# Performance work log

Measured on AMD Instinct MI355X. Metric: run time of the kernel, lower is better.

## Reference

```python
import jax, jax.numpy as jnp
import numpy as np
from jax import lax

DN = ('NCHW', 'OIHW', 'NCHW')
EPS = 1e-5


def _conv3x3(x, w, b):
    return lax.conv_general_dilated(x, w, (1, 1), 'SAME', dimension_numbers=DN) + b[:, None, None]


def _conv1x1(x, w, b):
    return jnp.einsum('bchw,oc->bohw', x, w) + b[:, None, None]


def _dwconv3x3(x, w, b):
    # w: (C,1,3,3), depthwise
    C = x.shape[1]
    return lax.conv_general_dilated(x, w, (1, 1), 'SAME', feature_group_count=C,
                                    dimension_numbers=DN) + b[:, None, None]


def setup_inputs() -> dict:
    key = jax.random.key(0)
    ks = jax.random.split(key, 24)
    b, t, c, h, w = 2, 8, 64, 160, 160
    r, K = c // 4, 3

    def n(k, shape, s=0.05):
        return jax.random.normal(k, shape, dtype=jnp.float32) * s

    return {
        'feature': n(ks[0], (b, t, c, h, w), 1.0),
        'kc_w1': n(ks[1], (r, c)),
        'kc_bn_gamma': jnp.ones((r,), jnp.float32),
        'kc_bn_beta': jnp.zeros((r,), jnp.float32),
        'kc_bn_mean': jnp.zeros((r,), jnp.float32),
        'kc_bn_var': jnp.ones((r,), jnp.float32),
        'kc_w2': n(ks[2], (c * K * K, r)),
        'kc_b2': n(ks[3], (c * K * K,)),
        'kc_bias': n(ks[4], (c,)),
        'conv1_w': n(ks[5], (2 * c, 2 * c, 3, 3)),
        'conv1_b': n(ks[6], (2 * c,)),
        'pi1_w': n(ks[7], (4 * c, c)),
        'pi1_b': n(ks[8], (4 * c,)),
        'dw1_w': n(ks[9], (4 * c, 1, 3, 3)),
        'dw1_b': n(ks[10], (4 * c,)),
        'po1_w': n(ks[11], (c, 4 * c)),
        'po1_b': n(ks[12], (c,)),
        'pi2_w': n(ks[13], (4 * c, c)),
        'pi2_b': n(ks[14], (4 * c,)),
        'dw2_w': n(ks[15], (4 * c, 1, 3, 3)),
        'dw2_b': n(ks[16], (4 * c,)),
        'po2_w': n(ks[17], (c, 4 * c)),
        'po2_b': n(ks[18], (c,)),
    }


def reference(feature, kc_w1, kc_bn_gamma, kc_bn_beta, kc_bn_mean, kc_bn_var,
              kc_w2, kc_b2, kc_bias, conv1_w, conv1_b,
              pi1_w, pi1_b, dw1_w, dw1_b, po1_w, po1_b,
              pi2_w, pi2_b, dw2_w, dw2_b, po2_w, po2_b):
    b, t, c, h, w = feature.shape
    K = int(round((kc_w2.shape[0] // c) ** 0.5))  # dynamic kernel size (3)

    def dyn_dwconv(x_feat, y):
        # kernel generation: GAP -> 1x1 -> BN(eval) -> ReLU -> 1x1
        pool = x_feat.mean(axis=(2, 3))                           # (b, c)
        z = pool @ kc_w1.T                                        # (b, r)
        z = (z - kc_bn_mean) * jax.lax.rsqrt(kc_bn_var + EPS) * kc_bn_gamma + kc_bn_beta
        z = jax.nn.relu(z)
        wd = (z @ kc_w2.T + kc_b2).reshape(b, c, K, K)            # per-sample dw kernels

        def per_sample(yi, wi):
            return lax.conv_general_dilated(yi[None], wi[:, None], (1, 1), 'SAME',
                                            feature_group_count=c,
                                            dimension_numbers=DN)[0]
        out = jax.vmap(per_sample)(y, wd)                         # (b, c, h, w)
        return out + kc_bias[None, :, None, None]

    def step(feat_prop, x_feat):
        fp = dyn_dwconv(x_feat, feat_prop)
        fusion = jnp.concatenate([x_feat, fp], axis=1)
        fusion = jax.nn.leaky_relu(_conv3x3(fusion, conv1_w, conv1_b), 0.1)
        f1, f2 = fusion[:, :c], fusion[:, c:]
        g1 = jax.nn.sigmoid(_conv1x1(_dwconv3x3(_conv1x1(f1, pi1_w, pi1_b), dw1_w, dw1_b), po1_w, po1_b))
        g2 = jax.nn.sigmoid(_conv1x1(_dwconv3x3(_conv1x1(f2, pi2_w, pi2_b), dw2_w, dw2_b), po2_w, po2_b))
        new_fp = f1 * g1 + f2 * g2
        return new_fp, new_fp

    init = feature[:, t - 1]                                      # frame t-1
    xs = jnp.moveaxis(jnp.flip(feature[:, :t - 1], axis=1), 1, 0)  # frames t-2 .. 0
    _, ys = lax.scan(step, init, xs)                              # (t-1, b, c, h, w)
    full = jnp.concatenate([jnp.flip(ys, axis=0), init[None]], axis=0)
    return jnp.moveaxis(full, 0, 1)                               # (b, t, c, h, w)
```

## Files before the change

### kernel.cpp

```cpp
#include <hip/hip_runtime.h>

typedef __attribute__((ext_vector_type(8))) __bf16 bf16x8;
typedef __attribute__((ext_vector_type(4))) float f32x4;
typedef __attribute__((ext_vector_type(2))) float f32x2;

#define BB 2
#define TT 8
#define CC 64
#define HH 160
#define WW 160
#define HWW 25600
#define RR 16
#define C2 128
#define C4 256
#define C8 512
#define NSTEP 7
#define CHW (CC*HWW)
#define EPSV 1e-5f

__device__ __forceinline__ f32x4 mfma16(bf16x8 a, bf16x8 b, f32x4 c) {
    return __builtin_amdgcn_mfma_f32_16x16x32_bf16(a, b, c, 0, 0, 0);
}

__device__ __forceinline__ void bpk_fma(unsigned d, f32x2 w, f32x2& a) {
    f32x2 u;
    u.x = __uint_as_float(d << 16);
    u.y = __uint_as_float(d & 0xffff0000u);
    a = __builtin_elementwise_fma(u, w, a);
}

__global__ void pool_kernel(const float* __restrict__ feat, float* __restrict__ pool) {
    int idx = blockIdx.x;
    int b = idx / (NSTEP * CC);
    int f = (idx / CC) % NSTEP;
    int c = idx % CC;
    const float4* src = (const float4*)(feat + ((size_t)(b * TT + f) * CC + c) * HWW);
    float s = 0.f;
    for (int i = threadIdx.x; i < HWW / 4; i += 256) {
        float4 v = src[i];
        s += v.x + v.y + v.z + v.w;
    }
    __shared__ float sm[256];
    sm[threadIdx.x] = s;
    __syncthreads();
    for (int off = 128; off > 0; off >>= 1) {
        if (threadIdx.x < off) sm[threadIdx.x] += sm[threadIdx.x + off];
        __syncthreads();
    }
    if (threadIdx.x == 0) pool[idx] = sm[0] * (1.0f / HWW);
}

__global__ void wd_kernel(const float* __restrict__ pool, const float* __restrict__ w1,
                          const float* __restrict__ gamma, const float* __restrict__ beta,
                          const float* __restrict__ mean, const float* __restrict__ var,
                          const float* __restrict__ w2, const float* __restrict__ b2,
                          float* __restrict__ wdT) {
    int bf = blockIdx.x;
    __shared__ float z[RR];
    int tid = threadIdx.x;
    if (tid < RR) {
        const float* p = pool + bf * CC;
        float s = 0.f;
        for (int c = 0; c < CC; c++) s += p[c] * w1[tid * CC + c];
        s = (s - mean[tid]) * rsqrtf(var[tid] + EPSV) * gamma[tid] + beta[tid];
        z[tid] = s > 0.f ? s : 0.f;
    }
    __syncthreads();
    for (int o = tid; o < CC * 9; o += 64) {
        float s = b2[o];
        #pragma unroll
        for (int r = 0; r < RR; r++) s += z[r] * w2[o * RR + r];
        int c = o / 9, t = o % 9;
        wdT[bf * 576 + t * CC + c] = s;
    }
}

__global__ void copy_init_kernel(const float* __restrict__ feat, float* __restrict__ out) {
    int i = blockIdx.x * 256 + threadIdx.x;
    int n4 = CHW / 4;
    int b = i / n4;
    int r = i % n4;
    size_t off = ((size_t)(b * TT + (TT - 1)) * CHW) / 4 + r;
    ((float4*)out)[off] = ((const float4*)feat)[off];
}

__global__ void prep_weights(const float* __restrict__ c1w,
                             const float* __restrict__ pi1, const float* __restrict__ pi2,
                             const float* __restrict__ po1, const float* __restrict__ po2,
                             const float* __restrict__ dw1, const float* __restrict__ dw2,
                             const float* __restrict__ dw1b, const float* __restrict__ dw2b,
                             __bf16* __restrict__ Bc1,
                             __bf16* __restrict__ Bpi1, __bf16* __restrict__ Bpi2,
                             __bf16* __restrict__ Bpo1, __bf16* __restrict__ Bpo2,
                             float* __restrict__ dwT12, float* __restrict__ dwb12,
                             __bf16* __restrict__ Bpk) {
    int idx = blockIdx.x * 256 + threadIdx.x;
    if (idx < 147456) {
        int oc = idx / 1152, k = idx % 1152;
        int t = k >> 7, ic = k & 127;
        Bc1[idx] = (__bf16)c1w[(oc * 128 + ic) * 9 + t];
        return;
    }
    idx -= 147456;
    if (idx < 16384) { Bpi1[idx] = (__bf16)pi1[idx]; return; }
    idx -= 16384;
    if (idx < 16384) { Bpi2[idx] = (__bf16)pi2[idx]; return; }
    idx -= 16384;
    if (idx < 16384) { Bpo1[idx] = (__bf16)po1[idx]; return; }
    idx -= 16384;
    if (idx < 16384) { Bpo2[idx] = (__bf16)po2[idx]; return; }
    idx -= 16384;
    if (idx < 4608) {
        int t = idx / 512, c = idx % 512;
        dwT12[t * C8 + c] = (c < 256) ? dw1[c * 9 + t] : dw2[(c - 256) * 9 + t];
        return;
    }
    idx -= 4608;
    if (idx < 512) { dwb12[idx] = (idx < 256) ? dw1b[idx] : dw2b[idx - 256]; return; }
    idx -= 512;
    if (idx < 32768) {
        int j = idx & 7, ln = (idx >> 3) & 63, nt = (idx >> 9) & 3, kg = (idx >> 11) & 3, cc = idx >> 13;
        int lmx = ln & 15, lqx = ln >> 4;
        int oc = nt * 16 + lmx;
        int ci = (cc & 1) * 128 + kg * 32 + lqx * 8 + j;
        const float* src = (cc >> 1) ? po2 : po1;
        Bpk[idx] = (__bf16)src[oc * C4 + ci];
    }
}

__global__ void featPM_kernel(const float* __restrict__ feat, __bf16* __restrict__ featPM) {
    __shared__ float Lt[64 * 68];
    int bf = blockIdx.x / 400;
    int p0 = (blockIdx.x % 400) * 64;
    int tid = threadIdx.x;
    int c = tid & 63, half = tid >> 6;
    const float* src = feat + ((size_t)bf * CC + c) * HWW + p0 + half * 16;
    #pragma unroll
    for (int k = 0; k < 16; k++) Lt[(half * 16 + k) * 68 + c] = src[k];
    __syncthreads();
    int cg = tid & 7;
    #pragma unroll
    for (int pass = 0; pass < 2; pass++) {
        int pl = (tid >> 3) + pass * 32;
        bf16x8 o;
        #pragma unroll
        for (int j = 0; j < 8; j++) o[j] = (__bf16)Lt[pl * 68 + cg * 8 + j];
        *(bf16x8*)(featPM + ((size_t)bf * HWW + p0 + pl) * CC + cg * 8) = o;
    }
}

__global__ void dyndw_kernel(const __bf16* __restrict__ src, size_t bstr,
                             const float* __restrict__ wdT, const float* __restrict__ kc_bias,
                             __bf16* __restrict__ fpPM, int fx) {
    int gi = blockIdx.x * 256 + threadIdx.x;
    int c0 = (gi & 7) * 8;
    int rem = gi >> 3;
    int p = rem % HWW;
    int bb = rem / HWW;
    int py = p / WW, px = p % WW;
    float acc[8];
    float4 k0 = *(const float4*)(kc_bias + c0);
    float4 k1 = *(const float4*)(kc_bias + c0 + 4);
    acc[0]=k0.x; acc[1]=k0.y; acc[2]=k0.z; acc[3]=k0.w;
    acc[4]=k1.x; acc[5]=k1.y; acc[6]=k1.z; acc[7]=k1.w;
    const float* wb = wdT + (size_t)(bb * NSTEP + fx) * 576;
    const __bf16* sb = src + (size_t)bb * bstr;
    const int dyA[9] = {-1,-1,-1,0,0,0,1,1,1};
    const int dxA[9] = {-1,0,1,-1,0,1,-1,0,1};
    #pragma unroll
    for (int t = 0; t < 9; t++) {
        int dy = dyA[t], dx = dxA[t];
        if ((unsigned)(py + dy) < HH && (unsigned)(px + dx) < WW) {
            bf16x8 uv = *(const bf16x8*)(sb + (size_t)(p + dy * WW + dx) * CC + c0);
            float4 w0 = *(const float4*)(wb + t * CC + c0);
            float4 w1 = *(const float4*)(wb + t * CC + c0 + 4);
            acc[0] += (float)uv[0] * w0.x; acc[1] += (float)uv[1] * w0.y;
            acc[2] += (float)uv[2] * w0.z; acc[3] += (float)uv[3] * w0.w;
            acc[4] += (float)uv[4] * w1.x; acc[5] += (float)uv[5] * w1.y;
            acc[6] += (float)uv[6] * w1.z; acc[7] += (float)uv[7] * w1.w;
        }
    }
    bf16x8 o;
    #pragma unroll
    for (int j = 0; j < 8; j++) o[j] = (__bf16)acc[j];
    *(bf16x8*)(fpPM + ((size_t)bb * HWW + p) * CC + c0) = o;
}

__global__ void conv1_gemm(const __bf16* __restrict__ featPM, const __bf16* __restrict__ fpPM,
                           const __bf16* __restrict__ Bc1, const float* __restrict__ bias,
                           __bf16* __restrict__ fusionPM, int fx) {
    __shared__ __align__(16) __bf16 As[128 * 40];
    __shared__ __align__(16) __bf16 Bs[128 * 40];
    const int tid = threadIdx.x;
    const int bid = blockIdx.x;
    const int wg = (bid & 7) * 50 + (bid >> 3);
    const int bb = wg / 200;
    const int p0 = (wg % 200) * 128;
    const int i = tid >> 1, h = tid & 1;
    const int p = p0 + i;
    const int py = p / WW, px = p % WW;
    const __bf16* featB = featPM + (size_t)(bb * TT + fx) * HWW * CC;
    const __bf16* fpB   = fpPM + (size_t)bb * HWW * CC;
    const int wv = tid >> 6, lane = tid & 63, lm = lane & 15, lq = lane >> 4;
    f32x4 acc[2][8];
    #pragma unroll
    for (int mt = 0; mt < 2; mt++)
        #pragma unroll
        for (int nt = 0; nt < 8; nt++) acc[mt][nt] = (f32x4){0.f, 0.f, 0.f, 0.f};

    for (int ks = 0; ks < 36; ks++) {
        const int t = ks >> 2, ci0 = (ks & 3) * 32;
        const int dy = t / 3 - 1, dx = t % 3 - 1;
        const bool valid = ((unsigned)(py + dy) < HH) && ((unsigned)(px + dx) < WW);
        uint4 a0 = {0,0,0,0}, a1 = {0,0,0,0};
        if (valid) {
            const __bf16* sp = (ci0 < 64)
                ? featB + (size_t)(p + dy * WW + dx) * CC + ci0
                : fpB   + (size_t)(p + dy * WW + dx) * CC + (ci0 - 64);
            a0 = *(const uint4*)(sp + h * 16);
            a1 = *(const uint4*)(sp + h * 16 + 8);
        }
        const __bf16* bp = Bc1 + (size_t)i * 1152 + ks * 32 + h * 16;
        uint4 w0q = *(const uint4*)(bp);
        uint4 w1q = *(const uint4*)(bp + 8);
        __syncthreads();
        *(uint4*)&As[i * 40 + h * 16]     = a0;
        *(uint4*)&As[i * 40 + h * 16 + 8] = a1;
        *(uint4*)&Bs[i * 40 + h * 16]     = w0q;
        *(uint4*)&Bs[i * 40 + h * 16 + 8] = w1q;
        __syncthreads();
        bf16x8 af0 = *(const bf16x8*)&As[((wv * 2 + 0) * 16 + lm) * 40 + lq * 8];
        bf16x8 af1 = *(const bf16x8*)&As[((wv * 2 + 1) * 16 + lm) * 40 + lq * 8];
        #pragma unroll
        for (int nt = 0; nt < 8; nt++) {
            bf16x8 bf = *(const bf16x8*)&Bs[(nt * 16 + lm) * 40 + lq * 8];
            acc[0][nt] = mfma16(af0, bf, acc[0][nt]);
            acc[1][nt] = mfma16(af1, bf, acc[1][nt]);
        }
    }
    __bf16* ob = fusionPM + (size_t)bb * HWW * C2;
    #pragma unroll
    for (int mt = 0; mt < 2; mt++) {
        #pragma unroll
        for (int nt = 0; nt < 8; nt++) {
            const int oc = nt * 16 + lm;
            const float bs = bias[oc];
            #pragma unroll
            for (int r = 0; r < 4; r++) {
                const int pp = p0 + (wv * 2 + mt) * 16 + lq * 4 + r;
                float v = acc[mt][nt][r] + bs;
                v = v > 0.f ? v : 0.1f * v;
                ob[(size_t)pp * C2 + oc] = (__bf16)v;
            }
        }
    }
}

__global__ void pw1_gemm(const __bf16* __restrict__ fusionPM,
                         const __bf16* __restrict__ Bpi1, const __bf16* __restrict__ Bpi2,
                         const float* __restrict__ pi1b, const float* __restrict__ pi2b,
                         __bf16* __restrict__ u12PM) {
    __shared__ __align__(16) __bf16 As[128 * 40];
    __shared__ __align__(16) __bf16 Bs[128 * 40];
    const int tid = threadIdx.x;
    const int bb = blockIdx.x / 800;
    const int rem = blockIdx.x % 800;
    const int p0 = (rem >> 2) * 128;
    const int nb = rem & 3;
    const int br = nb >> 1, ns = nb & 1;
    const __bf16* Bpi = br ? Bpi2 : Bpi1;
    const float* bias = br ? pi2b : pi1b;
    const int i = tid >> 1, h = tid & 1;
    const int p = p0 + i;
    const __bf16* fB = fusionPM + (size_t)bb * HWW * C2 + br * CC;
    const int wv = tid >> 6, lane = tid & 63, lm = lane & 15, lq = lane >> 4;
    f32x4 acc[2][8];
    #pragma unroll
    for (int mt = 0; mt < 2; mt++)
        #pragma unroll
        for (int nt = 0; nt < 8; nt++) acc[mt][nt] = (f32x4){0.f, 0.f, 0.f, 0.f};

    #pragma unroll
    for (int ks = 0; ks < 2; ks++) {
        const int ci0 = ks * 32;
        const __bf16* sp = fB + (size_t)p * C2 + ci0 + h * 16;
        uint4 a0 = *(const uint4*)(sp);
        uint4 a1 = *(const uint4*)(sp + 8);
        const __bf16* bp = Bpi + (size_t)(ns * 128 + i) * 64 + ci0 + h * 16;
        uint4 w0q = *(const uint4*)(bp);
        uint4 w1q = *(const uint4*)(bp + 8);
        __syncthreads();
        *(uint4*)&As[i * 40 + h * 16]     = a0;
        *(uint4*)&As[i * 40 + h * 16 + 8] = a1;
        *(uint4*)&Bs[i * 40 + h * 16]     = w0q;
        *(uint4*)&Bs[i * 40 + h * 16 + 8] = w1q;
        __syncthreads();
        bf16x8 af0 = *(const bf16x8*)&As[((wv * 2 + 0) * 16 + lm) * 40 + lq * 8];
        bf16x8 af1 = *(const bf16x8*)&As[((wv * 2 + 1) * 16 + lm) * 40 + lq * 8];
        #pragma unroll
        for (int nt = 0; nt < 8; nt++) {
            bf16x8 bf = *(const bf16x8*)&Bs[(nt * 16 + lm) * 40 + lq * 8];
            acc[0][nt] = mfma16(af0, bf, acc[0][nt]);
            acc[1][nt] = mfma16(af1, bf, acc[1][nt]);
        }
    }
    __bf16* ub = u12PM + (size_t)bb * HWW * C8;
    #pragma unroll
    for (int mt = 0; mt < 2; mt++) {
        #pragma unroll
        for (int nt = 0; nt < 8; nt++) {
            const int ocl = ns * 128 + nt * 16 + lm;
            const int oc = br * 256 + ocl;
            const float bs = bias[ocl];
            #pragma unroll
            for (int r = 0; r < 4; r++) {
                const int pp = p0 + (wv * 2 + mt) * 16 + lq * 4 + r;
                ub[(size_t)pp * C8 + oc] = (__bf16)(acc[mt][nt][r] + bs);
            }
        }
    }
}

__global__ void dwpw2_gemm(const __bf16* __restrict__ u12PM,
                           const float* __restrict__ dwT12, const float* __restrict__ dwb12,
                           const __bf16* __restrict__ Bpk,
                           const float* __restrict__ pob1, const float* __restrict__ pob2,
                           const __bf16* __restrict__ fusionPM,
                           float* __restrict__ out, __bf16* __restrict__ outPM, int fx) {
    __shared__ __align__(16) __bf16 uL[3 * 34 * 128];
    __shared__ __align__(16) __bf16 Vt[32 * 136];
    const int tid = threadIdx.x;
    const int bid = blockIdx.x;
    const int wg = (bid & 7) * 200 + (bid >> 3);
    const int bb = wg / 800;
    const int p0 = (wg % 800) * 32;
    const int py = p0 / WW, px0 = p0 % WW;
    const __bf16* uB = u12PM + (size_t)bb * HWW * C8;
    const int wv = tid >> 6, lane = tid & 63, lm = lane & 15, lq = lane >> 4;
    const int mt = wv & 1, nh = wv >> 1;
    const int cg = tid & 15, prow = tid >> 4;

    f32x4 acc[2][2];
    #pragma unroll
    for (int b = 0; b < 2; b++)
        #pragma unroll
        for (int n = 0; n < 2; n++) acc[b][n] = (f32x4){0.f, 0.f, 0.f, 0.f};

    const int rbase = py - 1, cbase = px0 - 1;

    #pragma unroll
    for (int cc = 0; cc < 4; cc++) {
        const int c0ch = cc * 128;
        #pragma unroll
        for (int it = 0; it < 7; it++) {
            int idx = it * 256 + tid;
            if (idx < 1632) {
                int s = idx >> 4, part = idx & 15;
                int r = s / 34, c = s - r * 34;
                int gr = rbase + r, gc = cbase + c;
                uint4 v = {0,0,0,0};
                if ((unsigned)gr < HH && (unsigned)gc < WW)
                    v = *(const uint4*)(uB + (size_t)(gr * WW + gc) * C8 + c0ch + part * 8);
                *(uint4*)&uL[idx * 8] = v;
            }
        }
        __syncthreads();

        const int c0 = c0ch + cg * 8;
        f32x2 a0[4], a1[4];
        {
            float4 b0 = *(const float4*)(dwb12 + c0);
            float4 b1 = *(const float4*)(dwb12 + c0 + 4);
            a0[0] = (f32x2){b0.x, b0.y}; a0[1] = (f32x2){b0.z, b0.w};
            a0[2] = (f32x2){b1.x, b1.y}; a0[3] = (f32x2){b1.z, b1.w};
            #pragma unroll
            for (int k = 0; k < 4; k++) a1[k] = a0[k];
        }
        #pragma unroll
        for (int t = 0; t < 9; t++) {
            const int dy = t / 3 - 1, dx = t % 3 - 1;
            float4 w0 = *(const float4*)(dwT12 + t * C8 + c0);
            float4 w1 = *(const float4*)(dwT12 + t * C8 + c0 + 4);
            f32x2 wp[4] = {(f32x2){w0.x, w0.y}, (f32x2){w0.z, w0.w},
                           (f32x2){w1.x, w1.y}, (f32x2){w1.z, w1.w}};
            const int base = ((1 + dy) * 34 + 1 + dx) * 128 + cg * 8;
            uint4 ua = *(const uint4*)&uL[base + prow * 128];
            uint4 ub4 = *(const uint4*)&uL[base + (prow + 16) * 128];
            bpk_fma(ua.x, wp[0], a0[0]); bpk_fma(ua.y, wp[1], a0[1]);
            bpk_fma(ua.z, wp[2], a0[2]); bpk_fma(ua.w, wp[3], a0[3]);
            bpk_fma(ub4.x, wp[0], a1[0]); bpk_fma(ub4.y, wp[1], a1[1]);
            bpk_fma(ub4.z, wp[2], a1[2]); bpk_fma(ub4.w, wp[3], a1[3]);
        }
        bf16x8 o0, o1;
        #pragma unroll
        for (int k = 0; k < 4; k++) {
            o0[2 * k] = (__bf16)a0[k].x; o0[2 * k + 1] = (__bf16)a0[k].y;
            o1[2 * k] = (__bf16)a1[k].x; o1[2 * k + 1] = (__bf16)a1[k].y;
        }
        *(bf16x8*)&Vt[prow * 136 + cg * 8]        = o0;
        *(bf16x8*)&Vt[(16 + prow) * 136 + cg * 8] = o1;
        __syncthreads();

        const int br = cc >> 1;
        const __bf16* bbase = Bpk + cc * 8192 + (size_t)lane * 8;
        #pragma unroll
        for (int kg = 0; kg < 4; kg++) {
            bf16x8 af = *(const bf16x8*)&Vt[(mt * 16 + lm) * 136 + kg * 32 + lq * 8];
            #pragma unroll
            for (int ntl = 0; ntl < 2; ntl++) {
                bf16x8 bfr = *(const bf16x8*)(bbase + kg * 2048 + (nh * 2 + ntl) * 512);
                acc[br][ntl] = mfma16(af, bfr, acc[br][ntl]);
            }
        }
    }
    const __bf16* fB = fusionPM + (size_t)bb * HWW * C2;
    __bf16* opB = outPM + (size_t)bb * HWW * CC;
    float* outp = out + (size_t)(bb * TT + fx) * CC * HWW;
    const int ppb = p0 + mt * 16 + lq * 4;
    #pragma unroll
    for (int ntl = 0; ntl < 2; ntl++) {
        const int oc = (nh * 2 + ntl) * 16 + lm;
        const float bs1 = pob1[oc];
        const float bs2 = pob2[oc];
        float4 vo;
        #pragma unroll
        for (int r = 0; r < 4; r++) {
            const int pp = ppb + r;
            float g1 = 1.f / (1.f + __expf(-(acc[0][ntl][r] + bs1)));
            float g2 = 1.f / (1.f + __expf(-(acc[1][ntl][r] + bs2)));
            float f1 = (float)fB[(size_t)pp * C2 + oc];
            float f2 = (float)fB[(size_t)pp * C2 + CC + oc];
            float val = f1 * g1 + f2 * g2;
            (&vo.x)[r] = val;
            opB[(size_t)pp * CC + oc] = (__bf16)val;
        }
        *(float4*)(outp + (size_t)oc * HWW + ppb) = vo;
    }
}

extern "C" void kernel_launch(void* const* d_in, const int* in_sizes, int n_in,
                              void* d_out, int out_size, void* d_ws, size_t ws_size,
                              hipStream_t stream) {
    const float* feat     = (const float*)d_in[0];
    const float* kc_w1    = (const float*)d_in[1];
    const float* kc_g     = (const float*)d_in[2];
    const float* kc_be    = (const float*)d_in[3];
    const float* kc_mu    = (const float*)d_in[4];
    const float* kc_var   = (const float*)d_in[5];
    const float* kc_w2    = (const float*)d_in[6];
    const float* kc_b2    = (const float*)d_in[7];
    const float* kc_bias  = (const float*)d_in[8];
    const float* conv1_w  = (const float*)d_in[9];
    const float* conv1_b  = (const float*)d_in[10];
    const float* pi1_w    = (const float*)d_in[11];
    const float* pi1_b    = (const float*)d_in[12];
    const float* dw1_w    = (const float*)d_in[13];
    const float* dw1_b    = (const float*)d_in[14];
    const float* po1_w    = (const float*)d_in[15];
    const float* po1_b    = (const float*)d_in[16];
    const float* pi2_w    = (const float*)d_in[17];
    const float* pi2_b    = (const float*)d_in[18];
    const float* dw2_w    = (const float*)d_in[19];
    const float* dw2_b    = (const float*)d_in[20];
    const float* po2_w    = (const float*)d_in[21];
    const float* po2_b    = (const float*)d_in[22];
    float* out = (float*)d_out;

    char* W = (char*)d_ws;
    __bf16* featPM   = (__bf16*)W; W += (size_t)BB * TT * HWW * CC * 2;
    __bf16* fpPM     = (__bf16*)W; W += (size_t)BB * HWW * CC * 2;
    __bf16* fusionPM = (__bf16*)W; W += (size_t)BB * HWW * C2 * 2;
    __bf16* u12PM    = (__bf16*)W; W += (size_t)BB * HWW * C8 * 2;
    __bf16* outPM    = (__bf16*)W; W += (size_t)BB * HWW * CC * 2;
    __bf16* Bc1      = (__bf16*)W; W += 294912;
    __bf16* Bpi1     = (__bf16*)W; W += 32768;
    __bf16* Bpi2     = (__bf16*)W; W += 32768;
    __bf16* Bpo1     = (__bf16*)W; W += 32768;
    __bf16* Bpo2     = (__bf16*)W; W += 32768;
    __bf16* Bpk      = (__bf16*)W; W += 65536;
    float*  dwT12    = (float*)W;  W += 18432;
    float*  dwb12    = (float*)W;  W += 2048;
    float*  poolb    = (float*)W;  W += 4096;
    float*  wdT      = (float*)W;  W += 32256;

    prep_weights<<<980, 256, 0, stream>>>(conv1_w, pi1_w, pi2_w, po1_w, po2_w, dw1_w, dw2_w,
                                          dw1_b, dw2_b,
                                          Bc1, Bpi1, Bpi2, Bpo1, Bpo2, dwT12, dwb12, Bpk);
    featPM_kernel<<<BB * TT * 400, 256, 0, stream>>>(feat, featPM);
    pool_kernel<<<BB * NSTEP * CC, 256, 0, stream>>>(feat, poolb);
    wd_kernel<<<BB * NSTEP, 64, 0, stream>>>(poolb, kc_w1, kc_g, kc_be, kc_mu, kc_var, kc_w2, kc_b2, wdT);
    copy_init_kernel<<<BB * CHW / 4 / 256, 256, 0, stream>>>(feat, out);

    for (int i = 0; i < NSTEP; i++) {
        int fx = NSTEP - 1 - i;
        const __bf16* src = (fx == NSTEP - 1) ? (featPM + (size_t)(TT - 1) * HWW * CC) : outPM;
        size_t bstr = (fx == NSTEP - 1) ? (size_t)TT * HWW * CC : (size_t)HWW * CC;
        dyndw_kernel<<<BB * HWW * 8 / 256, 256, 0, stream>>>(src, bstr, wdT, kc_bias, fpPM, fx);
        conv1_gemm<<<BB * 200, 256, 0, stream>>>(featPM, fpPM, Bc1, conv1_b, fusionPM, fx);
        pw1_gemm<<<BB * 800, 256, 0, stream>>>(fusionPM, Bpi1, Bpi2, pi1_b, pi2_b, u12PM);
        dwpw2_gemm<<<BB * 800, 256, 0, stream>>>(u12PM, dwT12, dwb12, Bpk, po1_b, po2_b, fusionPM, out, outPM, fx);
    }
}
```

Baseline: 1.006 ms.

## Tile conv1 as 2D spatial blocks with shared-memory halo and prepacked MFMA weights

```diff
diff --git a/kernel.cpp b/kernel.cpp
--- a/kernel.cpp
+++ b/kernel.cpp
@@ -96,8 +96,10 @@
                              __bf16* __restrict__ Bpk) {
     int idx = blockIdx.x * 256 + threadIdx.x;
     if (idx < 147456) {
-        int oc = idx / 1152, k = idx % 1152;
-        int t = k >> 7, ic = k & 127;
+        int j = idx & 7, ln = (idx >> 3) & 63, nt = (idx >> 9) & 7, ks = idx >> 12;
+        int lm = ln & 15, lq = ln >> 4;
+        int oc = nt * 16 + lm;
+        int t = ks >> 2, ic = (ks & 3) * 32 + lq * 8 + j;
         Bc1[idx] = (__bf16)c1w[(oc * 128 + ic) * 9 + t];
         return;
     }
@@ -187,67 +189,77 @@
 }
 
 __global__ void conv1_gemm(const __bf16* __restrict__ featPM, const __bf16* __restrict__ fpPM,
-                           const __bf16* __restrict__ Bc1, const float* __restrict__ bias,
+                           const __bf16* __restrict__ Bpkc, const float* __restrict__ bias,
                            __bf16* __restrict__ fusionPM, int fx) {
-    __shared__ __align__(16) __bf16 As[128 * 40];
-    __shared__ __align__(16) __bf16 Bs[128 * 40];
+    __shared__ __align__(16) __bf16 uA[10 * 18 * 136];
     const int tid = threadIdx.x;
     const int bid = blockIdx.x;
     const int wg = (bid & 7) * 50 + (bid >> 3);
     const int bb = wg / 200;
-    const int p0 = (wg % 200) * 128;
-    const int i = tid >> 1, h = tid & 1;
-    const int p = p0 + i;
-    const int py = p / WW, px = p % WW;
+    const int rem = wg % 200;
+    const int r0 = (rem / 10) * 8, c0 = (rem % 10) * 16;
     const __bf16* featB = featPM + (size_t)(bb * TT + fx) * HWW * CC;
     const __bf16* fpB   = fpPM + (size_t)bb * HWW * CC;
     const int wv = tid >> 6, lane = tid & 63, lm = lane & 15, lq = lane >> 4;
+
+    #pragma unroll
+    for (int it = 0; it < 12; it++) {
+        int idx = it * 256 + tid;
+        if (idx < 2880) {
+            int s = idx >> 4, part = idx & 15;
+            int r = s / 18, c = s % 18;
+            int gr = r0 - 1 + r, gc = c0 - 1 + c;
+            uint4 v = {0, 0, 0, 0};
+            if ((unsigned)gr < HH && (unsigned)gc < WW) {
+                const __bf16* sp = (part < 8)
+                    ? featB + (size_t)(gr * WW + gc) * CC + part * 8
+                    : fpB   + (size_t)(gr * WW + gc) * CC + (part - 8) * 8;
+                v = *(const uint4*)sp;
+            }
+            *(uint4*)&uA[(r * 18 + c) * 136 + part * 8] = v;
+        }
+    }
+    __syncthreads();
+
     f32x4 acc[2][8];
     #pragma unroll
     for (int mt = 0; mt < 2; mt++)
         #pragma unroll
         for (int nt = 0; nt < 8; nt++) acc[mt][nt] = (f32x4){0.f, 0.f, 0.f, 0.f};
 
-    for (int ks = 0; ks < 36; ks++) {
-        const int t = ks >> 2, ci0 = (ks & 3) * 32;
-        const int dy = t / 3 - 1, dx = t % 3 - 1;
-        const bool valid = ((unsigned)(py + dy) < HH) && ((unsigned)(px + dx) < WW);
-        uint4 a0 = {0,0,0,0}, a1 = {0,0,0,0};
-        if (valid) {
-            const __bf16* sp = (ci0 < 64)
-                ? featB + (size_t)(p + dy * WW + dx) * CC + ci0
-                : fpB   + (size_t)(p + dy * WW + dx) * CC + (ci0 - 64);
-            a0 = *(const uint4*)(sp + h * 16);
-            a1 = *(const uint4*)(sp + h * 16 + 8);
-        }
-        const __bf16* bp = Bc1 + (size_t)i * 1152 + ks * 32 + h * 16;
-        uint4 w0q = *(const uint4*)(bp);
-        uint4 w1q = *(const uint4*)(bp + 8);
-        __syncthreads();
-        *(uint4*)&As[i * 40 + h * 16]     = a0;
-        *(uint4*)&As[i * 40 + h * 16 + 8] = a1;
-        *(uint4*)&Bs[i * 40 + h * 16]     = w0q;
-        *(uint4*)&Bs[i * 40 + h * 16 + 8] = w1q;
-        __syncthreads();
-        bf16x8 af0 = *(const bf16x8*)&As[((wv * 2 + 0) * 16 + lm) * 40 + lq * 8];
-        bf16x8 af1 = *(const bf16x8*)&As[((wv * 2 + 1) * 16 + lm) * 40 + lq * 8];
-        #pragma unroll
-        for (int nt = 0; nt < 8; nt++) {
-            bf16x8 bf = *(const bf16x8*)&Bs[(nt * 16 + lm) * 40 + lq * 8];
-            acc[0][nt] = mfma16(af0, bf, acc[0][nt]);
-            acc[1][nt] = mfma16(af1, bf, acc[1][nt]);
+    const __bf16* bp0 = Bpkc + (size_t)lane * 8;
+    const int dyA[9] = {-1,-1,-1,0,0,0,1,1,1};
+    const int dxA[9] = {-1,0,1,-1,0,1,-1,0,1};
+    #pragma unroll
+    for (int t = 0; t < 9; t++) {
+        const int arow = wv * 2 + 1 + dyA[t];
+        const int acol = lm + 1 + dxA[t];
+        const int abase = (arow * 18 + acol) * 136;
+        #pragma unroll
+        for (int kc = 0; kc < 4; kc++) {
+            const int ks = t * 4 + kc;
+            bf16x8 af0 = *(const bf16x8*)&uA[abase + kc * 32 + lq * 8];
+            bf16x8 af1 = *(const bf16x8*)&uA[abase + 18 * 136 + kc * 32 + lq * 8];
+            const __bf16* bks = bp0 + (size_t)ks * 4096;
+            #pragma unroll
+            for (int nt = 0; nt < 8; nt++) {
+                bf16x8 bfr = *(const bf16x8*)(bks + nt * 512);
+                acc[0][nt] = mfma16(af0, bfr, acc[0][nt]);
+                acc[1][nt] = mfma16(af1, bfr, acc[1][nt]);
+            }
         }
     }
     __bf16* ob = fusionPM + (size_t)bb * HWW * C2;
     #pragma unroll
     for (int mt = 0; mt < 2; mt++) {
+        const int prow = r0 + wv * 2 + mt;
         #pragma unroll
         for (int nt = 0; nt < 8; nt++) {
             const int oc = nt * 16 + lm;
             const float bs = bias[oc];
             #pragma unroll
             for (int r = 0; r < 4; r++) {
-                const int pp = p0 + (wv * 2 + mt) * 16 + lq * 4 + r;
+                const int pp = prow * WW + c0 + lq * 4 + r;
                 float v = acc[mt][nt][r] + bs;
                 v = v > 0.f ? v : 0.1f * v;
                 ob[(size_t)pp * C2 + oc] = (__bf16)v;
```

Result: slower. 1.314 ms (+30.6%).
